# Kernel tuning notes

Hardware: AMD Instinct MI355X
Metric: run time of the kernel (lower is better)

The kernel has to match this reference:

```python
import jax, jax.numpy as jnp
import numpy as np

B, TAPE, N, F = 128, 100000, 50000, 32

def setup_inputs() -> dict:
    key = jax.random.key(0)
    k1, k2, k3, k4 = jax.random.split(key, 4)
    tape = jax.random.normal(k1, (B, TAPE), dtype=jnp.float32)
    input_indices = jax.random.randint(k2, (N, F), 0, TAPE)
    # He init scaled by fan-in, padding slots (index==0) zeroed as in __init__
    weights = jax.random.normal(k3, (N, F), dtype=jnp.float32) * jnp.sqrt(2.0 / F)
    weights = jnp.where(input_indices == 0, 0.0, weights)
    bias = jnp.zeros((N,), dtype=jnp.float32)
    output_indices = jnp.arange(N)
    act_type = jax.random.randint(k4, (N,), 0, 2)
    return {"tape": tape, "weights": weights, "bias": bias,
            "input_indices": input_indices, "output_indices": output_indices,
            "act_type": act_type}

def reference(tape, weights, bias, input_indices, output_indices, act_type):
    # gather padded fan-in inputs: [B, N, F]
    gathered = tape[:, input_indices]
    # weighted sum over fan-in + bias: [B, N]
    x = jnp.einsum('bnf,nf->bn', gathered, weights) + bias
    # per-activation-type apply (two activation groups: relu / tanh)
    x = jnp.where(act_type == 0, jax.nn.relu(x), jnp.tanh(x))
    # scatter results back into tape
    return tape.at[:, output_indices].set(x)
```

## Files before the change

kernel.cpp:

```cpp
#include <hip/hip_runtime.h>
#include <cmath>

#define TAPE_SZ 100000
#define N_SZ    50000
#define F_SZ    32
#define B_SZ    128
#define NGRP    8
#define GSUB    16
#define NBV     64
#define NCHUNK  ((N_SZ + NBV - 1) / NBV)
#define NGATHER (NCHUNK * NGRP)
#define NTAIL   512
#define TAIL_F4 1600000

static __device__ __forceinline__ unsigned short f32_to_bf16(float f) {
    unsigned int u = __float_as_uint(f);
    u = (u + 0x7fffu + ((u >> 16) & 1u)) >> 16;
    return (unsigned short)u;
}

__global__ __launch_bounds__(256) void transpose_tape(const float* __restrict__ in,
                                                      unsigned short* __restrict__ outT) {
    __shared__ float tile[32][129];
    const int x0 = blockIdx.x * 32;
    const int tx = threadIdx.x;
    const int ty = threadIdx.y;

    #pragma unroll
    for (int yy = ty; yy < B_SZ; yy += 8)
        tile[tx][yy] = in[(size_t)yy * TAPE_SZ + x0 + tx];
    __syncthreads();

    const int tid = ty * 32 + tx;
    const int g = tid >> 5;
    const int l = tid & 31;
    unsigned short* dst = outT + ((size_t)g * TAPE_SZ + x0 + l) * GSUB;
    union { unsigned short u[8]; uint4 q; } p0, p1;
    #pragma unroll
    for (int k = 0; k < 8; ++k) {
        p0.u[k] = f32_to_bf16(tile[l][g * GSUB + k]);
        p1.u[k] = f32_to_bf16(tile[l][g * GSUB + 8 + k]);
    }
    *(uint4*)dst       = p0.q;
    *(uint4*)(dst + 8) = p1.q;
}

__global__ __launch_bounds__(256, 8) void gather_mm(const unsigned short* __restrict__ tapeT,
                                                    const float* __restrict__ weights,
                                                    const float* __restrict__ bias,
                                                    const int*   __restrict__ in_idx,
                                                    const int*   __restrict__ out_idx,
                                                    const int*   __restrict__ act_type,
                                                    const float* __restrict__ tape,
                                                    float* __restrict__ out) {
    __shared__ int2  s_iw[NBV][33];
    __shared__ float s_bias[NBV];
    __shared__ int   s_act[NBV];
    __shared__ int   s_oidx[NBV];
    float (*s_x)[68] = (float (*)[68])&s_iw[0][0];

    const int tid = threadIdx.x;

    if (blockIdx.x >= NGATHER) {
        const float4* src = (const float4*)tape;
        float4*       dst = (float4*)out;
        const int stride = NTAIL * 256;
        for (int i = (blockIdx.x - NGATHER) * 256 + tid; i < TAIL_F4; i += stride) {
            const int b = i / 12500;
            const int j = i - b * 12500;
            const int off = b * (TAPE_SZ / 4) + (N_SZ / 4) + j;
            dst[off] = src[off];
        }
        return;
    }

    const int g     = blockIdx.x & (NGRP - 1);
    const int chunk = blockIdx.x >> 3;
    const int n0    = chunk * NBV;
    const int nend  = min(NBV, N_SZ - n0);

    for (int t = tid; t < nend * 32; t += 256) {
        const int n = t >> 5, f = t & 31;
        s_iw[n][f] = make_int2(in_idx[(size_t)n0 * 32 + t],
                               __float_as_int(weights[(size_t)n0 * 32 + t]));
    }
    if (tid < nend) {
        s_bias[tid] = bias[n0 + tid];
        s_act[tid]  = act_type[n0 + tid];
        s_oidx[tid] = out_idx[n0 + tid];
    }
    __syncthreads();

    const int nl = tid >> 2;
    const int q  = tid & 3;
    const unsigned short* tg = tapeT + (size_t)g * TAPE_SZ * GSUB + q * 4;

    float a0 = 0.f, a1 = 0.f, a2 = 0.f, a3 = 0.f;
    if (nl < nend) {
        #pragma unroll
        for (int fo = 0; fo < 32; fo += 8) {
            int2 iw8[8];
            #pragma unroll
            for (int j = 0; j < 8; ++j) iw8[j] = s_iw[nl][fo + j];
            uint2 q8[8];
            #pragma unroll
            for (int j = 0; j < 8; ++j)
                q8[j] = *(const uint2*)(tg + (size_t)iw8[j].x * GSUB);
            #pragma unroll
            for (int j = 0; j < 8; ++j) {
                const float w = __int_as_float(iw8[j].y);
                a0 = fmaf(__uint_as_float(q8[j].x << 16),         w, a0);
                a1 = fmaf(__uint_as_float(q8[j].x & 0xffff0000u), w, a1);
                a2 = fmaf(__uint_as_float(q8[j].y << 16),         w, a2);
                a3 = fmaf(__uint_as_float(q8[j].y & 0xffff0000u), w, a3);
            }
        }
        const float bz = s_bias[nl];
        a0 += bz; a1 += bz; a2 += bz; a3 += bz;
        if (s_act[nl] == 0) {
            a0 = fmaxf(a0, 0.f); a1 = fmaxf(a1, 0.f);
            a2 = fmaxf(a2, 0.f); a3 = fmaxf(a3, 0.f);
        } else {
            a0 = tanhf(a0); a1 = tanhf(a1); a2 = tanhf(a2); a3 = tanhf(a3);
        }
    }
    __syncthreads();

    if (nl < nend) {
        const int bs = q * 4;
        s_x[bs + 0][nl] = a0; s_x[bs + 1][nl] = a1;
        s_x[bs + 2][nl] = a2; s_x[bs + 3][nl] = a3;
    }
    __syncthreads();

    const int quads = (nend + 3) >> 2;
    for (int idx = tid; idx < GSUB * quads; idx += 256) {
        int bsub, j4;
        if (nend == NBV) { bsub = idx >> 4; j4 = idx & 15; }
        else             { bsub = idx / quads; j4 = idx - bsub * quads; }
        const int nq  = j4 * 4;
        const int oc0 = s_oidx[nq];
        float* orow = out + (size_t)(g * GSUB + bsub) * TAPE_SZ;
        const bool consec = (nq + 3 < nend) &&
                            (s_oidx[nq + 1] == oc0 + 1) &&
                            (s_oidx[nq + 2] == oc0 + 2) &&
                            (s_oidx[nq + 3] == oc0 + 3) && ((oc0 & 3) == 0);
        if (consec) {
            *(float4*)(orow + oc0) = make_float4(s_x[bsub][nq + 0], s_x[bsub][nq + 1],
                                                 s_x[bsub][nq + 2], s_x[bsub][nq + 3]);
        } else {
            #pragma unroll
            for (int c = 0; c < 4; ++c)
                if (nq + c < nend) orow[s_oidx[nq + c]] = s_x[bsub][nq + c];
        }
    }
}

__global__ __launch_bounds__(128) void gather_fallback(const float* __restrict__ tape,
                                                       const float* __restrict__ weights,
                                                       const float* __restrict__ bias,
                                                       const int*   __restrict__ in_idx,
                                                       const int*   __restrict__ out_idx,
                                                       const int*   __restrict__ act_type,
                                                       float* __restrict__ out) {
    const int n = blockIdx.x;
    const int b = threadIdx.x;
    float acc = 0.f;
    for (int f = 0; f < F_SZ; ++f) {
        acc += tape[(size_t)b * TAPE_SZ + in_idx[(size_t)n * F_SZ + f]] *
               weights[(size_t)n * F_SZ + f];
    }
    acc += bias[n];
    acc = (act_type[n] == 0) ? fmaxf(acc, 0.f) : tanhf(acc);
    out[(size_t)b * TAPE_SZ + out_idx[n]] = acc;
}

__global__ __launch_bounds__(256) void copy_tail_fb(const float* __restrict__ tape,
                                                    float* __restrict__ out) {
    const int n4 = (TAPE_SZ - N_SZ) / 4;
    int i = blockIdx.x * blockDim.x + threadIdx.x;
    int b = blockIdx.y;
    if (i < n4) {
        const float4* src = (const float4*)(tape + (size_t)b * TAPE_SZ + N_SZ);
        float4*       dst = (float4*)(out  + (size_t)b * TAPE_SZ + N_SZ);
        dst[i] = src[i];
    }
}

extern "C" void kernel_launch(void* const* d_in, const int* in_sizes, int n_in,
                              void* d_out, int out_size, void* d_ws, size_t ws_size,
                              hipStream_t stream) {
    const float* tape    = (const float*)d_in[0];
    const float* weights = (const float*)d_in[1];
    const float* bias    = (const float*)d_in[2];
    const int*   in_idx  = (const int*)d_in[3];
    const int*   out_idx = (const int*)d_in[4];
    const int*   act     = (const int*)d_in[5];
    float*       out     = (float*)d_out;

    const size_t need = (size_t)TAPE_SZ * B_SZ * sizeof(unsigned short);
    if (ws_size >= need) {
        unsigned short* tapeT = (unsigned short*)d_ws;
        transpose_tape<<<dim3(TAPE_SZ / 32), dim3(32, 8), 0, stream>>>(tape, tapeT);
        gather_mm<<<dim3(NGATHER + NTAIL), dim3(256), 0, stream>>>(
            tapeT, weights, bias, in_idx, out_idx, act, tape, out);
    } else {
        copy_tail_fb<<<dim3(((TAPE_SZ - N_SZ) / 4 + 255) / 256, B_SZ), 256, 0, stream>>>(tape, out);
        gather_fallback<<<dim3(N_SZ), 128, 0, stream>>>(
            tape, weights, bias, in_idx, out_idx, act, out);
    }
}
```

Baseline: 187.8 us.

## Add full-batch bf16 tape layout and split neurons between two gather schemes

The transpose now writes two bf16 copies of the tape: the existing batch-grouped layout and a neuron-major layout holding all 128 batch entries per tape slot. Neurons below a split point keep the grouped 64-neuron scheme. The rest use a new 16-neuron-per-block scheme that reads 16-byte full-batch rows with nontemporal loads and interleaves block types in the grid. The tail copy uses nontemporal loads and stores. The aim is to balance gather traffic and cut redundant index and weight loads, at the cost of a second transpose write, twice the workspace, and a hard-coded split ratio.

```diff
diff --git a/kernel.cpp b/kernel.cpp
--- a/kernel.cpp
+++ b/kernel.cpp
@@ -7,11 +7,19 @@
 #define B_SZ    128
 #define NGRP    8
 #define GSUB    16
+
 #define NBV     64
-#define NCHUNK  ((N_SZ + NBV - 1) / NBV)
-#define NGATHER (NCHUNK * NGRP)
+#define N_SPLIT 30016
+#define NCHA    (N_SPLIT / NBV)
+#define NB_B    16
+#define NBLK_B  ((N_SZ - N_SPLIT) / NB_B)
+#define NPER    157
+#define NMAIN   (NPER * 4 * 8)
 #define NTAIL   512
 #define TAIL_F4 1600000
+
+typedef float        f32x4 __attribute__((ext_vector_type(4)));
+typedef unsigned int u32x4 __attribute__((ext_vector_type(4)));
 
 static __device__ __forceinline__ unsigned short f32_to_bf16(float f) {
     unsigned int u = __float_as_uint(f);
@@ -19,8 +27,9 @@
     return (unsigned short)u;
 }
 
-__global__ __launch_bounds__(256) void transpose_tape(const float* __restrict__ in,
-                                                      unsigned short* __restrict__ outT) {
+__global__ __launch_bounds__(256) void transpose_both(const float* __restrict__ in,
+                                                      unsigned short* __restrict__ outP,
+                                                      unsigned short* __restrict__ outF) {
     __shared__ float tile[32][129];
     const int x0 = blockIdx.x * 32;
     const int tx = threadIdx.x;
@@ -32,76 +41,106 @@
     __syncthreads();
 
     const int tid = ty * 32 + tx;
-    const int g = tid >> 5;
-    const int l = tid & 31;
-    unsigned short* dst = outT + ((size_t)g * TAPE_SZ + x0 + l) * GSUB;
-    union { unsigned short u[8]; uint4 q; } p0, p1;
-    #pragma unroll
-    for (int k = 0; k < 8; ++k) {
-        p0.u[k] = f32_to_bf16(tile[l][g * GSUB + k]);
-        p1.u[k] = f32_to_bf16(tile[l][g * GSUB + 8 + k]);
-    }
-    *(uint4*)dst       = p0.q;
-    *(uint4*)(dst + 8) = p1.q;
-}
-
-__global__ __launch_bounds__(256, 8) void gather_mm(const unsigned short* __restrict__ tapeT,
-                                                    const float* __restrict__ weights,
-                                                    const float* __restrict__ bias,
-                                                    const int*   __restrict__ in_idx,
-                                                    const int*   __restrict__ out_idx,
-                                                    const int*   __restrict__ act_type,
-                                                    const float* __restrict__ tape,
-                                                    float* __restrict__ out) {
-    __shared__ int2  s_iw[NBV][33];
-    __shared__ float s_bias[NBV];
-    __shared__ int   s_act[NBV];
-    __shared__ int   s_oidx[NBV];
-    float (*s_x)[68] = (float (*)[68])&s_iw[0][0];
-
+    {
+        const int g = tid >> 5, l = tid & 31;
+        unsigned short* dst = outP + ((size_t)g * TAPE_SZ + x0 + l) * GSUB;
+        union { unsigned short u[8]; uint4 q; } p0, p1;
+        #pragma unroll
+        for (int k = 0; k < 8; ++k) {
+            p0.u[k] = f32_to_bf16(tile[l][g * GSUB + k]);
+            p1.u[k] = f32_to_bf16(tile[l][g * GSUB + 8 + k]);
+        }
+        *(uint4*)dst       = p0.q;
+        *(uint4*)(dst + 8) = p1.q;
+    }
+    {
+        const int l = tid >> 3, o = tid & 7;
+        unsigned short* dst = outF + (size_t)(x0 + l) * B_SZ + o * 8;
+        union { unsigned short u[8]; uint4 q; } p0, p1;
+        #pragma unroll
+        for (int k = 0; k < 8; ++k) {
+            p0.u[k] = f32_to_bf16(tile[l][o * 8 + k]);
+            p1.u[k] = f32_to_bf16(tile[l][64 + o * 8 + k]);
+        }
+        *(uint4*)dst        = p0.q;
+        *(uint4*)(dst + 64) = p1.q;
+    }
+}
+
+union SMem {
+    struct {
+        int2  iw[NBV][33];
+        float bias[NBV];
+        int   act[NBV];
+        int   oidx[NBV];
+    } a;
+    float ax[GSUB][68];
+    struct {
+        int   idx[NB_B][33];
+        float w[NB_B][33];
+        float x[NB_B][132];
+        float bias[NB_B];
+        int   act[NB_B];
+        int   oidx[NB_B];
+    } b;
+};
+
+__global__ __launch_bounds__(256) void gather_mm(const unsigned short* __restrict__ tapeP,
+                                                 const unsigned short* __restrict__ tapeF,
+                                                 const float* __restrict__ weights,
+                                                 const float* __restrict__ bias,
+                                                 const int*   __restrict__ in_idx,
+                                                 const int*   __restrict__ out_idx,
+                                                 const int*   __restrict__ act_type,
+                                                 const float* __restrict__ tape,
+                                                 float* __restrict__ out) {
+    __shared__ SMem sm;
     const int tid = threadIdx.x;
 
-    if (blockIdx.x >= NGATHER) {
-        const float4* src = (const float4*)tape;
-        float4*       dst = (float4*)out;
+    if (blockIdx.x >= NMAIN) {
         const int stride = NTAIL * 256;
-        for (int i = (blockIdx.x - NGATHER) * 256 + tid; i < TAIL_F4; i += stride) {
-            const int b = i / 12500;
-            const int j = i - b * 12500;
-            const int off = b * (TAPE_SZ / 4) + (N_SZ / 4) + j;
-            dst[off] = src[off];
+        for (int i = (blockIdx.x - NMAIN) * 256 + tid; i < TAIL_F4; i += stride) {
+            const int bb = i / 12500;
+            const int j = i - bb * 12500;
+            const size_t off = (size_t)bb * (TAPE_SZ / 4) + (N_SZ / 4) + j;
+            f32x4 v = __builtin_nontemporal_load((const f32x4*)tape + off);
+            __builtin_nontemporal_store(v, (f32x4*)out + off);
         }
         return;
     }
 
-    const int g     = blockIdx.x & (NGRP - 1);
-    const int chunk = blockIdx.x >> 3;
-    const int n0    = chunk * NBV;
-    const int nend  = min(NBV, N_SZ - n0);
-
-    for (int t = tid; t < nend * 32; t += 256) {
-        const int n = t >> 5, f = t & 31;
-        s_iw[n][f] = make_int2(in_idx[(size_t)n0 * 32 + t],
-                               __float_as_int(weights[(size_t)n0 * 32 + t]));
-    }
-    if (tid < nend) {
-        s_bias[tid] = bias[n0 + tid];
-        s_act[tid]  = act_type[n0 + tid];
-        s_oidx[tid] = out_idx[n0 + tid];
-    }
-    __syncthreads();
-
-    const int nl = tid >> 2;
-    const int q  = tid & 3;
-    const unsigned short* tg = tapeT + (size_t)g * TAPE_SZ * GSUB + q * 4;
-
-    float a0 = 0.f, a1 = 0.f, a2 = 0.f, a3 = 0.f;
-    if (nl < nend) {
+    const int oct = blockIdx.x >> 3;
+    const int g   = blockIdx.x & 7;
+    const int po  = oct & 3;
+    const int ro  = oct >> 2;
+
+    if (po < 3) {
+        const int chunk = ro * 3 + po;
+        if (chunk >= NCHA) return;
+        const int n0 = chunk * NBV;
+
+        for (int t = tid; t < NBV * 32; t += 256) {
+            const int n = t >> 5, f = t & 31;
+            sm.a.iw[n][f] = make_int2(in_idx[(size_t)n0 * 32 + t],
+                                      __float_as_int(weights[(size_t)n0 * 32 + t]));
+        }
+        if (tid < NBV) {
+            sm.a.bias[tid] = bias[n0 + tid];
+            sm.a.act[tid]  = act_type[n0 + tid];
+            sm.a.oidx[tid] = out_idx[n0 + tid];
+        }
+        __syncthreads();
+
+        const int nl = tid >> 2;
+        const int q  = tid & 3;
+        const unsigned short* tg = tapeP + (size_t)g * TAPE_SZ * GSUB + q * 4;
+
+        float a0 = 0.f, a1 = 0.f, a2 = 0.f, a3 = 0.f;
         #pragma unroll
         for (int fo = 0; fo < 32; fo += 8) {
             int2 iw8[8];
             #pragma unroll
-            for (int j = 0; j < 8; ++j) iw8[j] = s_iw[nl][fo + j];
+            for (int j = 0; j < 8; ++j) iw8[j] = sm.a.iw[nl][fo + j];
             uint2 q8[8];
             #pragma unroll
             for (int j = 0; j < 8; ++j)
@@ -115,6 +154,216 @@
                 a3 = fmaf(__uint_as_float(q8[j].y & 0xffff0000u), w, a3);
             }
         }
+        const float bz = sm.a.bias[nl];
+        a0 += bz; a1 += bz; a2 += bz; a3 += bz;
+        if (sm.a.act[nl] == 0) {
+            a0 = fmaxf(a0, 0.f); a1 = fmaxf(a1, 0.f);
+            a2 = fmaxf(a2, 0.f); a3 = fmaxf(a3, 0.f);
+        } else {
+            a0 = tanhf(a0); a1 = tanhf(a1); a2 = tanhf(a2); a3 = tanhf(a3);
+        }
+        __syncthreads();
+
+        {
+            const int bs = q * 4;
+            sm.ax[bs + 0][nl] = a0; sm.ax[bs + 1][nl] = a1;
+            sm.ax[bs + 2][nl] = a2; sm.ax[bs + 3][nl] = a3;
+        }
+        __syncthreads();
+
+        for (int idx = tid; idx < GSUB * 16; idx += 256) {
+            const int bsub = idx >> 4, j4 = idx & 15;
+            const int nq  = j4 * 4;
+            const int oc0 = sm.a.oidx[nq];
+            float* orow = out + (size_t)(g * GSUB + bsub) * TAPE_SZ;
+            const bool consec = (sm.a.oidx[nq + 1] == oc0 + 1) &&
+                                (sm.a.oidx[nq + 2] == oc0 + 2) &&
+                                (sm.a.oidx[nq + 3] == oc0 + 3) && ((oc0 & 3) == 0);
+            if (consec) {
+                *(float4*)(orow + oc0) = make_float4(sm.ax[bsub][nq + 0], sm.ax[bsub][nq + 1],
+                                                     sm.ax[bsub][nq + 2], sm.ax[bsub][nq + 3]);
+            } else {
+                #pragma unroll
+                for (int c = 0; c < 4; ++c)
+                    orow[sm.a.oidx[nq + c]] = sm.ax[bsub][nq + c];
+            }
+        }
+        return;
+    }
+
+    const int bidx = ro * 8 + g;
+    if (bidx >= NBLK_B) return;
+    const int n0 = N_SPLIT + bidx * NB_B;
+
+    for (int t = tid; t < NB_B * 32; t += 256) {
+        const int n = t >> 5, f = t & 31;
+        sm.b.idx[n][f] = in_idx[(size_t)n0 * 32 + t];
+        sm.b.w[n][f]   = weights[(size_t)n0 * 32 + t];
+    }
+    if (tid < NB_B) {
+        sm.b.bias[tid] = bias[n0 + tid];
+        sm.b.act[tid]  = act_type[n0 + tid];
+        sm.b.oidx[tid] = out_idx[n0 + tid];
+    }
+    __syncthreads();
+
+    const int nl = tid >> 4;
+    const int bx = tid & 15;
+    const unsigned short* tf = tapeF + bx * 8;
+    float a0 = 0.f, a1 = 0.f, a2 = 0.f, a3 = 0.f, a4 = 0.f, a5 = 0.f, a6 = 0.f, a7 = 0.f;
+
+    #pragma unroll
+    for (int fo = 0; fo < 32; fo += 8) {
+        int   i8[8]; float w8[8];
+        #pragma unroll
+        for (int j = 0; j < 8; ++j) { i8[j] = sm.b.idx[nl][fo + j]; w8[j] = sm.b.w[nl][fo + j]; }
+        u32x4 q8[8];
+        #pragma unroll
+        for (int j = 0; j < 8; ++j)
+            q8[j] = __builtin_nontemporal_load((const u32x4*)(tf + (size_t)i8[j] * B_SZ));
+        #pragma unroll
+        for (int j = 0; j < 8; ++j) {
+            const float w = w8[j];
+            a0 = fmaf(__uint_as_float(q8[j][0] << 16),         w, a0);
+            a1 = fmaf(__uint_as_float(q8[j][0] & 0xffff0000u), w, a1);
+            a2 = fmaf(__uint_as_float(q8[j][1] << 16),         w, a2);
+            a3 = fmaf(__uint_as_float(q8[j][1] & 0xffff0000u), w, a3);
+            a4 = fmaf(__uint_as_float(q8[j][2] << 16),         w, a4);
+            a5 = fmaf(__uint_as_float(q8[j][2] & 0xffff0000u), w, a5);
+            a6 = fmaf(__uint_as_float(q8[j][3] << 16),         w, a6);
+            a7 = fmaf(__uint_as_float(q8[j][3] & 0xffff0000u), w, a7);
+        }
+    }
+
+    const float bz = sm.b.bias[nl];
+    a0 += bz; a1 += bz; a2 += bz; a3 += bz; a4 += bz; a5 += bz; a6 += bz; a7 += bz;
+    if (sm.b.act[nl] == 0) {
+        a0 = fmaxf(a0, 0.f); a1 = fmaxf(a1, 0.f); a2 = fmaxf(a2, 0.f); a3 = fmaxf(a3, 0.f);
+        a4 = fmaxf(a4, 0.f); a5 = fmaxf(a5, 0.f); a6 = fmaxf(a6, 0.f); a7 = fmaxf(a7, 0.f);
+    } else {
+        a0 = tanhf(a0); a1 = tanhf(a1); a2 = tanhf(a2); a3 = tanhf(a3);
+        a4 = tanhf(a4); a5 = tanhf(a5); a6 = tanhf(a6); a7 = tanhf(a7);
+    }
+    {
+        const int b8 = bx * 8;
+        sm.b.x[nl][b8 + 0] = a0; sm.b.x[nl][b8 + 1] = a1; sm.b.x[nl][b8 + 2] = a2; sm.b.x[nl][b8 + 3] = a3;
+        sm.b.x[nl][b8 + 4] = a4; sm.b.x[nl][b8 + 5] = a5; sm.b.x[nl][b8 + 6] = a6; sm.b.x[nl][b8 + 7] = a7;
+    }
+    __syncthreads();
+
+    const int g4 = tid >> 6;
+    const int b0 = tid & 63;
+    const int oc0 = sm.b.oidx[g4 * 4];
+    const bool consec = (sm.b.oidx[g4 * 4 + 1] == oc0 + 1) &&
+                        (sm.b.oidx[g4 * 4 + 2] == oc0 + 2) &&
+                        (sm.b.oidx[g4 * 4 + 3] == oc0 + 3) && ((oc0 & 3) == 0);
+    #pragma unroll
+    for (int rep = 0; rep < 2; ++rep) {
+        const int b = b0 + rep * 64;
+        const float4 v = make_float4(sm.b.x[g4 * 4 + 0][b], sm.b.x[g4 * 4 + 1][b],
+                                     sm.b.x[g4 * 4 + 2][b], sm.b.x[g4 * 4 + 3][b]);
+        if (consec) {
+            *(float4*)(out + (size_t)b * TAPE_SZ + oc0) = v;
+        } else {
+            out[(size_t)b * TAPE_SZ + sm.b.oidx[g4 * 4 + 0]] = v.x;
+            out[(size_t)b * TAPE_SZ + sm.b.oidx[g4 * 4 + 1]] = v.y;
+            out[(size_t)b * TAPE_SZ + sm.b.oidx[g4 * 4 + 2]] = v.z;
+            out[(size_t)b * TAPE_SZ + sm.b.oidx[g4 * 4 + 3]] = v.w;
+        }
+    }
+}
+
+#define NBV2    64
+#define NCHUNK2 ((N_SZ + NBV2 - 1) / NBV2)
+#define NGATH2  (NCHUNK2 * NGRP)
+
+__global__ __launch_bounds__(256) void transpose_part(const float* __restrict__ in,
+                                                      unsigned short* __restrict__ outT) {
+    __shared__ float tile[32][129];
+    const int x0 = blockIdx.x * 32;
+    const int tx = threadIdx.x, ty = threadIdx.y;
+    #pragma unroll
+    for (int yy = ty; yy < B_SZ; yy += 8)
+        tile[tx][yy] = in[(size_t)yy * TAPE_SZ + x0 + tx];
+    __syncthreads();
+    const int tid = ty * 32 + tx;
+    const int g = tid >> 5, l = tid & 31;
+    unsigned short* dst = outT + ((size_t)g * TAPE_SZ + x0 + l) * GSUB;
+    union { unsigned short u[8]; uint4 q; } p0, p1;
+    #pragma unroll
+    for (int k = 0; k < 8; ++k) {
+        p0.u[k] = f32_to_bf16(tile[l][g * GSUB + k]);
+        p1.u[k] = f32_to_bf16(tile[l][g * GSUB + 8 + k]);
+    }
+    *(uint4*)dst = p0.q; *(uint4*)(dst + 8) = p1.q;
+}
+
+__global__ __launch_bounds__(256, 8) void gather_mm_part(const unsigned short* __restrict__ tapeT,
+                                                         const float* __restrict__ weights,
+                                                         const float* __restrict__ bias,
+                                                         const int*   __restrict__ in_idx,
+                                                         const int*   __restrict__ out_idx,
+                                                         const int*   __restrict__ act_type,
+                                                         const float* __restrict__ tape,
+                                                         float* __restrict__ out) {
+    __shared__ int2  s_iw[NBV2][33];
+    __shared__ float s_bias[NBV2];
+    __shared__ int   s_act[NBV2];
+    __shared__ int   s_oidx[NBV2];
+    float (*s_x)[68] = (float (*)[68])&s_iw[0][0];
+    const int tid = threadIdx.x;
+
+    if (blockIdx.x >= NGATH2) {
+        const float4* src = (const float4*)tape;
+        float4*       dst = (float4*)out;
+        const int stride = NTAIL * 256;
+        for (int i = (blockIdx.x - NGATH2) * 256 + tid; i < TAIL_F4; i += stride) {
+            const int b = i / 12500;
+            const int j = i - b * 12500;
+            const int off = b * (TAPE_SZ / 4) + (N_SZ / 4) + j;
+            dst[off] = src[off];
+        }
+        return;
+    }
+    const int g = blockIdx.x & (NGRP - 1);
+    const int chunk = blockIdx.x >> 3;
+    const int n0 = chunk * NBV2;
+    const int nend = min(NBV2, N_SZ - n0);
+
+    for (int t = tid; t < nend * 32; t += 256) {
+        const int n = t >> 5, f = t & 31;
+        s_iw[n][f] = make_int2(in_idx[(size_t)n0 * 32 + t],
+                               __float_as_int(weights[(size_t)n0 * 32 + t]));
+    }
+    if (tid < nend) {
+        s_bias[tid] = bias[n0 + tid];
+        s_act[tid]  = act_type[n0 + tid];
+        s_oidx[tid] = out_idx[n0 + tid];
+    }
+    __syncthreads();
+
+    const int nl = tid >> 2, q = tid & 3;
+    const unsigned short* tg = tapeT + (size_t)g * TAPE_SZ * GSUB + q * 4;
+    float a0 = 0.f, a1 = 0.f, a2 = 0.f, a3 = 0.f;
+    if (nl < nend) {
+        #pragma unroll
+        for (int fo = 0; fo < 32; fo += 8) {
+            int2 iw8[8];
+            #pragma unroll
+            for (int j = 0; j < 8; ++j) iw8[j] = s_iw[nl][fo + j];
+            uint2 q8[8];
+            #pragma unroll
+            for (int j = 0; j < 8; ++j)
+                q8[j] = *(const uint2*)(tg + (size_t)iw8[j].x * GSUB);
+            #pragma unroll
+            for (int j = 0; j < 8; ++j) {
+                const float w = __int_as_float(iw8[j].y);
+                a0 = fmaf(__uint_as_float(q8[j].x << 16),         w, a0);
+                a1 = fmaf(__uint_as_float(q8[j].x & 0xffff0000u), w, a1);
+                a2 = fmaf(__uint_as_float(q8[j].y << 16),         w, a2);
+                a3 = fmaf(__uint_as_float(q8[j].y & 0xffff0000u), w, a3);
+            }
+        }
         const float bz = s_bias[nl];
         a0 += bz; a1 += bz; a2 += bz; a3 += bz;
         if (s_act[nl] == 0) {
@@ -125,25 +374,22 @@
         }
     }
     __syncthreads();
-
     if (nl < nend) {
         const int bs = q * 4;
         s_x[bs + 0][nl] = a0; s_x[bs + 1][nl] = a1;
         s_x[bs + 2][nl] = a2; s_x[bs + 3][nl] = a3;
     }
     __syncthreads();
-
     const int quads = (nend + 3) >> 2;
     for (int idx = tid; idx < GSUB * quads; idx += 256) {
         int bsub, j4;
-        if (nend == NBV) { bsub = idx >> 4; j4 = idx & 15; }
-        else             { bsub = idx / quads; j4 = idx - bsub * quads; }
-        const int nq  = j4 * 4;
+        if (nend == NBV2) { bsub = idx >> 4; j4 = idx & 15; }
+        else              { bsub = idx / quads; j4 = idx - bsub * quads; }
+        const int nq = j4 * 4;
         const int oc0 = s_oidx[nq];
         float* orow = out + (size_t)(g * GSUB + bsub) * TAPE_SZ;
         const bool consec = (nq + 3 < nend) &&
-                            (s_oidx[nq + 1] == oc0 + 1) &&
-                            (s_oidx[nq + 2] == oc0 + 2) &&
+                            (s_oidx[nq + 1] == oc0 + 1) && (s_oidx[nq + 2] == oc0 + 2) &&
                             (s_oidx[nq + 3] == oc0 + 3) && ((oc0 & 3) == 0);
         if (consec) {
             *(float4*)(orow + oc0) = make_float4(s_x[bsub][nq + 0], s_x[bsub][nq + 1],
@@ -198,11 +444,17 @@
     const int*   act     = (const int*)d_in[5];
     float*       out     = (float*)d_out;
 
-    const size_t need = (size_t)TAPE_SZ * B_SZ * sizeof(unsigned short);
-    if (ws_size >= need) {
+    const size_t one = (size_t)TAPE_SZ * B_SZ * sizeof(unsigned short);
+    if (ws_size >= 2 * one) {
+        unsigned short* tapeP = (unsigned short*)d_ws;
+        unsigned short* tapeF = tapeP + (size_t)TAPE_SZ * B_SZ;
+        transpose_both<<<dim3(TAPE_SZ / 32), dim3(32, 8), 0, stream>>>(tape, tapeP, tapeF);
+        gather_mm<<<dim3(NMAIN + NTAIL), dim3(256), 0, stream>>>(
+            tapeP, tapeF, weights, bias, in_idx, out_idx, act, tape, out);
+    } else if (ws_size >= one) {
         unsigned short* tapeT = (unsigned short*)d_ws;
-        transpose_tape<<<dim3(TAPE_SZ / 32), dim3(32, 8), 0, stream>>>(tape, tapeT);
-        gather_mm<<<dim3(NGATHER + NTAIL), dim3(256), 0, stream>>>(
+        transpose_part<<<dim3(TAPE_SZ / 32), dim3(32, 8), 0, stream>>>(tape, tapeT);
+        gather_mm_part<<<dim3(NGATH2 + NTAIL), dim3(256), 0, stream>>>(
             tapeT, weights, bias, in_idx, out_idx, act, tape, out);
     } else {
         copy_tail_fb<<<dim3(((TAPE_SZ - N_SZ) / 4 + 255) / 256, B_SZ), 256, 0, stream>>>(tape, out);
```

Result: slower. 204.5 us (+8.9%).

## Add cooperative phased gather kernel with tape-range sorted indices and grid syncs

Applied to the files above, without the earlier changes.

Adds a new path that transposes the tape into a row-major bf16 layout (128 batch values per tape column), then launches a cooperative kernel. Each block sorts its neurons' fan-in indices into four tape-index ranges and processes one range at a time, with grid-wide syncs between ranges, so all blocks touch the same quarter of the table together and that quarter can stay in cache. Each thread now loads 64 contiguous bytes per index and accumulates 32 batch values, and the tail copy is folded into the same kernel. The cost is three grid barriers, heavy register use (32 accumulators, 4 blocks/CU) and a 782-block grid that must be fully co-resident; the kernel falls back to the old path if the cooperative launch fails.

```diff
diff --git a/kernel.cpp b/kernel.cpp
--- a/kernel.cpp
+++ b/kernel.cpp
@@ -1,15 +1,17 @@
 #include <hip/hip_runtime.h>
+#include <hip/hip_cooperative_groups.h>
 #include <cmath>
+
+namespace cg = cooperative_groups;
 
 #define TAPE_SZ 100000
 #define N_SZ    50000
 #define F_SZ    32
 #define B_SZ    128
-#define NGRP    8
-#define GSUB    16
-#define NBV     64
-#define NCHUNK  ((N_SZ + NBV - 1) / NBV)
-#define NGATHER (NCHUNK * NGRP)
+#define RANGE   25000
+#define NBV     128
+#define NCHUNK  391
+#define GRID_G  (NCHUNK*2)
 #define NTAIL   512
 #define TAIL_F4 1600000
 
@@ -19,8 +21,8 @@
     return (unsigned short)u;
 }
 
-__global__ __launch_bounds__(256) void transpose_tape(const float* __restrict__ in,
-                                                      unsigned short* __restrict__ outT) {
+__global__ __launch_bounds__(256) void transpose_full(const float* __restrict__ in,
+                                                      unsigned short* __restrict__ outF) {
     __shared__ float tile[32][129];
     const int x0 = blockIdx.x * 32;
     const int tx = threadIdx.x;
@@ -32,8 +34,184 @@
     __syncthreads();
 
     const int tid = ty * 32 + tx;
-    const int g = tid >> 5;
-    const int l = tid & 31;
+    const int l = tid >> 3, o = tid & 7;
+    unsigned short* dst = outF + (size_t)(x0 + l) * B_SZ + o * 8;
+    union { unsigned short u[8]; uint4 q; } p0, p1;
+    #pragma unroll
+    for (int k = 0; k < 8; ++k) {
+        p0.u[k] = f32_to_bf16(tile[l][o * 8 + k]);
+        p1.u[k] = f32_to_bf16(tile[l][64 + o * 8 + k]);
+    }
+    *(uint4*)dst        = p0.q;
+    *(uint4*)(dst + 64) = p1.q;
+}
+
+__global__ __launch_bounds__(256, 4) void gather_phased(
+    const unsigned short* __restrict__ tapeF,
+    const float* __restrict__ weights,
+    const float* __restrict__ bias,
+    const int*   __restrict__ in_idx,
+    const int*   __restrict__ out_idx,
+    const int*   __restrict__ act_type,
+    const float* __restrict__ tape,
+    float* __restrict__ out) {
+    __shared__ union {
+        struct {
+            uint2 ent[NBV][33];
+            int   start[NBV][5];
+        } s;
+        float x[64][132];
+    } u;
+    __shared__ int   s_oidx[NBV];
+    __shared__ float s_bias[NBV];
+    __shared__ int   s_act[NBV];
+
+    const int tid   = threadIdx.x;
+    const int h     = blockIdx.x & 1;
+    const int chunk = blockIdx.x >> 1;
+    const int n0    = chunk * NBV;
+    const int nend  = min(NBV, N_SZ - n0);
+
+    if (tid < NBV) {
+        if (tid < nend) {
+            const int*   ip = in_idx  + (size_t)(n0 + tid) * 32;
+            const float* wp = weights + (size_t)(n0 + tid) * 32;
+            int ix[32];
+            #pragma unroll
+            for (int f = 0; f < 32; ++f) ix[f] = ip[f];
+            int c0 = 0, c1 = 0, c2 = 0, c3 = 0;
+            #pragma unroll
+            for (int f = 0; f < 32; ++f) {
+                const int r = ix[f] / RANGE;
+                c0 += (r == 0); c1 += (r == 1); c2 += (r == 2); c3 += (r == 3);
+            }
+            int o0 = 0, o1 = c0, o2 = c0 + c1, o3 = c0 + c1 + c2;
+            u.s.start[tid][0] = 0;  u.s.start[tid][1] = o1;
+            u.s.start[tid][2] = o2; u.s.start[tid][3] = o3;
+            u.s.start[tid][4] = 32;
+            #pragma unroll
+            for (int f = 0; f < 32; ++f) {
+                const int r = ix[f] / RANGE;
+                int pos;
+                if      (r == 0) pos = o0++;
+                else if (r == 1) pos = o1++;
+                else if (r == 2) pos = o2++;
+                else             pos = o3++;
+                u.s.ent[tid][pos] = make_uint2((unsigned)ix[f], __float_as_uint(wp[f]));
+            }
+            s_oidx[tid] = out_idx[n0 + tid];
+            s_bias[tid] = bias[n0 + tid];
+            s_act[tid]  = act_type[n0 + tid];
+        } else {
+            #pragma unroll
+            for (int r = 0; r < 5; ++r) u.s.start[tid][r] = 0;
+        }
+    }
+    __syncthreads();
+
+    const int nl = tid >> 1;
+    const int bq = tid & 1;
+    const unsigned short* tg = tapeF + h * 64 + bq * 32;
+
+    float a[32];
+    #pragma unroll
+    for (int j = 0; j < 32; ++j) a[j] = 0.f;
+
+    cg::grid_group grid = cg::this_grid();
+
+    #pragma unroll 1
+    for (int r = 0; r < 4; ++r) {
+        const int e0 = u.s.start[nl][r];
+        const int e1 = u.s.start[nl][r + 1];
+        for (int e = e0; e < e1; ++e) {
+            const uint2 iw = u.s.ent[nl][e];
+            const unsigned short* p = tg + (size_t)iw.x * B_SZ;
+            const uint4 q0 = *(const uint4*)(p +  0);
+            const uint4 q1 = *(const uint4*)(p +  8);
+            const uint4 q2 = *(const uint4*)(p + 16);
+            const uint4 q3 = *(const uint4*)(p + 24);
+            const float wv = __uint_as_float(iw.y);
+#define ACC8(Q, B0) \
+            a[B0+0] = fmaf(__uint_as_float((Q).x << 16),          wv, a[B0+0]); \
+            a[B0+1] = fmaf(__uint_as_float((Q).x & 0xffff0000u),  wv, a[B0+1]); \
+            a[B0+2] = fmaf(__uint_as_float((Q).y << 16),          wv, a[B0+2]); \
+            a[B0+3] = fmaf(__uint_as_float((Q).y & 0xffff0000u),  wv, a[B0+3]); \
+            a[B0+4] = fmaf(__uint_as_float((Q).z << 16),          wv, a[B0+4]); \
+            a[B0+5] = fmaf(__uint_as_float((Q).z & 0xffff0000u),  wv, a[B0+5]); \
+            a[B0+6] = fmaf(__uint_as_float((Q).w << 16),          wv, a[B0+6]); \
+            a[B0+7] = fmaf(__uint_as_float((Q).w & 0xffff0000u),  wv, a[B0+7]);
+            ACC8(q0, 0) ACC8(q1, 8) ACC8(q2, 16) ACC8(q3, 24)
+#undef ACC8
+        }
+        if (r < 3) grid.sync();
+    }
+
+    {
+        const float bz = (nl < nend) ? s_bias[nl] : 0.f;
+        const int   at = (nl < nend) ? s_act[nl]  : 0;
+        #pragma unroll
+        for (int j = 0; j < 32; ++j) {
+            const float v = a[j] + bz;
+            a[j] = (at == 0) ? fmaxf(v, 0.f) : tanhf(v);
+        }
+    }
+    __syncthreads();
+    if (nl < nend) {
+        #pragma unroll
+        for (int j = 0; j < 32; ++j)
+            u.x[bq * 32 + j][nl] = a[j];
+    }
+    __syncthreads();
+
+    const int quads = (nend + 3) >> 2;
+    for (int it = tid; it < 64 * quads; it += 256) {
+        int bsub, j4;
+        if (nend == NBV) { bsub = it >> 5; j4 = it & 31; }
+        else             { bsub = it / quads; j4 = it - bsub * quads; }
+        const int nq  = j4 * 4;
+        const int oc0 = s_oidx[nq];
+        float* orow = out + (size_t)(h * 64 + bsub) * TAPE_SZ;
+        const bool consec = (nq + 3 < nend) &&
+                            (s_oidx[nq + 1] == oc0 + 1) &&
+                            (s_oidx[nq + 2] == oc0 + 2) &&
+                            (s_oidx[nq + 3] == oc0 + 3) && ((oc0 & 3) == 0);
+        if (consec) {
+            *(float4*)(orow + oc0) = *(const float4*)&u.x[bsub][nq];
+        } else {
+            #pragma unroll
+            for (int c = 0; c < 4; ++c)
+                if (nq + c < nend) orow[s_oidx[nq + c]] = u.x[bsub][nq + c];
+        }
+    }
+
+    {
+        const int stride = GRID_G * 256;
+        for (int i = blockIdx.x * 256 + tid; i < TAIL_F4; i += stride) {
+            const int bb = i / 12500;
+            const int j  = i - bb * 12500;
+            const size_t off = (size_t)bb * (TAPE_SZ / 4) + (N_SZ / 4) + j;
+            ((float4*)out)[off] = ((const float4*)tape)[off];
+        }
+    }
+}
+
+#define NGRP    8
+#define GSUB    16
+#define NBV2    64
+#define NCHUNK2 ((N_SZ + NBV2 - 1) / NBV2)
+#define NGATH2  (NCHUNK2 * NGRP)
+
+__global__ __launch_bounds__(256) void transpose_part(const float* __restrict__ in,
+                                                      unsigned short* __restrict__ outT) {
+    __shared__ float tile[32][129];
+    const int x0 = blockIdx.x * 32;
+    const int tx = threadIdx.x, ty = threadIdx.y;
+    #pragma unroll
+    for (int yy = ty; yy < B_SZ; yy += 8)
+        tile[tx][yy] = in[(size_t)yy * TAPE_SZ + x0 + tx];
+    __syncthreads();
+    const int tid = ty * 32 + tx;
+    const int g = tid >> 5, l = tid & 31;
     unsigned short* dst = outT + ((size_t)g * TAPE_SZ + x0 + l) * GSUB;
     union { unsigned short u[8]; uint4 q; } p0, p1;
     #pragma unroll
@@ -41,31 +219,29 @@
         p0.u[k] = f32_to_bf16(tile[l][g * GSUB + k]);
         p1.u[k] = f32_to_bf16(tile[l][g * GSUB + 8 + k]);
     }
-    *(uint4*)dst       = p0.q;
-    *(uint4*)(dst + 8) = p1.q;
-}
-
-__global__ __launch_bounds__(256, 8) void gather_mm(const unsigned short* __restrict__ tapeT,
-                                                    const float* __restrict__ weights,
-                                                    const float* __restrict__ bias,
-                                                    const int*   __restrict__ in_idx,
-                                                    const int*   __restrict__ out_idx,
-                                                    const int*   __restrict__ act_type,
-                                                    const float* __restrict__ tape,
-                                                    float* __restrict__ out) {
-    __shared__ int2  s_iw[NBV][33];
-    __shared__ float s_bias[NBV];
-    __shared__ int   s_act[NBV];
-    __shared__ int   s_oidx[NBV];
+    *(uint4*)dst = p0.q; *(uint4*)(dst + 8) = p1.q;
+}
+
+__global__ __launch_bounds__(256, 8) void gather_mm_part(const unsigned short* __restrict__ tapeT,
+                                                         const float* __restrict__ weights,
+                                                         const float* __restrict__ bias,
+                                                         const int*   __restrict__ in_idx,
+                                                         const int*   __restrict__ out_idx,
+                                                         const int*   __restrict__ act_type,
+                                                         const float* __restrict__ tape,
+                                                         float* __restrict__ out) {
+    __shared__ int2  s_iw[NBV2][33];
+    __shared__ float s_bias[NBV2];
+    __shared__ int   s_act[NBV2];
+    __shared__ int   s_oidx[NBV2];
     float (*s_x)[68] = (float (*)[68])&s_iw[0][0];
-
     const int tid = threadIdx.x;
 
-    if (blockIdx.x >= NGATHER) {
+    if (blockIdx.x >= NGATH2) {
         const float4* src = (const float4*)tape;
         float4*       dst = (float4*)out;
         const int stride = NTAIL * 256;
-        for (int i = (blockIdx.x - NGATHER) * 256 + tid; i < TAIL_F4; i += stride) {
+        for (int i = (blockIdx.x - NGATH2) * 256 + tid; i < TAIL_F4; i += stride) {
             const int b = i / 12500;
             const int j = i - b * 12500;
             const int off = b * (TAPE_SZ / 4) + (N_SZ / 4) + j;
@@ -73,11 +249,10 @@
         }
         return;
     }
-
-    const int g     = blockIdx.x & (NGRP - 1);
+    const int g = blockIdx.x & (NGRP - 1);
     const int chunk = blockIdx.x >> 3;
-    const int n0    = chunk * NBV;
-    const int nend  = min(NBV, N_SZ - n0);
+    const int n0 = chunk * NBV2;
+    const int nend = min(NBV2, N_SZ - n0);
 
     for (int t = tid; t < nend * 32; t += 256) {
         const int n = t >> 5, f = t & 31;
@@ -91,10 +266,8 @@
     }
     __syncthreads();
 
-    const int nl = tid >> 2;
-    const int q  = tid & 3;
+    const int nl = tid >> 2, q = tid & 3;
     const unsigned short* tg = tapeT + (size_t)g * TAPE_SZ * GSUB + q * 4;
-
     float a0 = 0.f, a1 = 0.f, a2 = 0.f, a3 = 0.f;
     if (nl < nend) {
         #pragma unroll
@@ -125,25 +298,22 @@
         }
     }
     __syncthreads();
-
     if (nl < nend) {
         const int bs = q * 4;
         s_x[bs + 0][nl] = a0; s_x[bs + 1][nl] = a1;
         s_x[bs + 2][nl] = a2; s_x[bs + 3][nl] = a3;
     }
     __syncthreads();
-
     const int quads = (nend + 3) >> 2;
     for (int idx = tid; idx < GSUB * quads; idx += 256) {
         int bsub, j4;
-        if (nend == NBV) { bsub = idx >> 4; j4 = idx & 15; }
-        else             { bsub = idx / quads; j4 = idx - bsub * quads; }
-        const int nq  = j4 * 4;
+        if (nend == NBV2) { bsub = idx >> 4; j4 = idx & 15; }
+        else              { bsub = idx / quads; j4 = idx - bsub * quads; }
+        const int nq = j4 * 4;
         const int oc0 = s_oidx[nq];
         float* orow = out + (size_t)(g * GSUB + bsub) * TAPE_SZ;
         const bool consec = (nq + 3 < nend) &&
-                            (s_oidx[nq + 1] == oc0 + 1) &&
-                            (s_oidx[nq + 2] == oc0 + 2) &&
+                            (s_oidx[nq + 1] == oc0 + 1) && (s_oidx[nq + 2] == oc0 + 2) &&
                             (s_oidx[nq + 3] == oc0 + 3) && ((oc0 & 3) == 0);
         if (consec) {
             *(float4*)(orow + oc0) = make_float4(s_x[bsub][nq + 0], s_x[bsub][nq + 1],
@@ -198,11 +368,25 @@
     const int*   act     = (const int*)d_in[5];
     float*       out     = (float*)d_out;
 
-    const size_t need = (size_t)TAPE_SZ * B_SZ * sizeof(unsigned short);
-    if (ws_size >= need) {
+    const size_t one = (size_t)TAPE_SZ * B_SZ * sizeof(unsigned short);
+    if (ws_size >= 2 * one) {
+        unsigned short* tapeF = (unsigned short*)d_ws;
+        transpose_full<<<dim3(TAPE_SZ / 32), dim3(32, 8), 0, stream>>>(tape, tapeF);
+        void* args[] = {(void*)&tapeF, (void*)&weights, (void*)&bias, (void*)&in_idx,
+                        (void*)&out_idx, (void*)&act, (void*)&tape, (void*)&out};
+        hipError_t e = hipLaunchCooperativeKernel((const void*)gather_phased,
+                                                  dim3(GRID_G), dim3(256),
+                                                  args, 0, stream);
+        if (e != hipSuccess) {
+            unsigned short* tapeP = tapeF + (size_t)TAPE_SZ * B_SZ;
+            transpose_part<<<dim3(TAPE_SZ / 32), dim3(32, 8), 0, stream>>>(tape, tapeP);
+            gather_mm_part<<<dim3(NGATH2 + NTAIL), dim3(256), 0, stream>>>(
+                tapeP, weights, bias, in_idx, out_idx, act, tape, out);
+        }
+    } else if (ws_size >= one) {
         unsigned short* tapeT = (unsigned short*)d_ws;
-        transpose_tape<<<dim3(TAPE_SZ / 32), dim3(32, 8), 0, stream>>>(tape, tapeT);
-        gather_mm<<<dim3(NGATHER + NTAIL), dim3(256), 0, stream>>>(
+        transpose_part<<<dim3(TAPE_SZ / 32), dim3(32, 8), 0, stream>>>(tape, tapeT);
+        gather_mm_part<<<dim3(NGATH2 + NTAIL), dim3(256), 0, stream>>>(
             tapeT, weights, bias, in_idx, out_idx, act, tape, out);
     } else {
         copy_tail_fb<<<dim3(((TAPE_SZ - N_SZ) / 4 + 255) / 256, B_SZ), 256, 0, stream>>>(tape, out);
```

After: 479.8 us. 156% more time.

## Widen batch groups to 64, bucket gather indices by tape range, fuse tail copy

Applied to the files above, without the earlier changes.

The bf16 transposed tape now groups 64 batch rows per tape column instead of 16, so each gathered index fetches 128 contiguous bytes and each thread accumulates 16 batch values. The gather kernel uses 512 threads and 128 nodes per block, and sorts each node's 32 fan-in entries into four tape-range buckets. All threads sweep the buckets in step with a barrier between them, which aims to improve L2 locality. The untouched tail columns are now copied from the transpose kernel's shared tile, so the separate tail-copy blocks are gone. In exchange the gather kernel needs more registers and extra barriers, and the fan-in is split across 4 rounds of scattered loads.

```diff
diff --git a/kernel.cpp b/kernel.cpp
--- a/kernel.cpp
+++ b/kernel.cpp
@@ -5,13 +5,11 @@
 #define N_SZ    50000
 #define F_SZ    32
 #define B_SZ    128
-#define NGRP    8
-#define GSUB    16
-#define NBV     64
-#define NCHUNK  ((N_SZ + NBV - 1) / NBV)
-#define NGATHER (NCHUNK * NGRP)
-#define NTAIL   512
-#define TAIL_F4 1600000
+#define GSUB    64
+#define RANGE   25000
+#define NBV     128
+#define NCHUNK  391
+#define GRID_G  (NCHUNK*2)
 
 static __device__ __forceinline__ unsigned short f32_to_bf16(float f) {
     unsigned int u = __float_as_uint(f);
@@ -19,8 +17,9 @@
     return (unsigned short)u;
 }
 
-__global__ __launch_bounds__(256) void transpose_tape(const float* __restrict__ in,
-                                                      unsigned short* __restrict__ outT) {
+__global__ __launch_bounds__(256) void transpose_g64(const float* __restrict__ in,
+                                                     unsigned short* __restrict__ outG,
+                                                     float* __restrict__ out) {
     __shared__ float tile[32][129];
     const int x0 = blockIdx.x * 32;
     const int tx = threadIdx.x;
@@ -32,112 +31,143 @@
     __syncthreads();
 
     const int tid = ty * 32 + tx;
-    const int g = tid >> 5;
-    const int l = tid & 31;
-    unsigned short* dst = outT + ((size_t)g * TAPE_SZ + x0 + l) * GSUB;
+    const int l = tid >> 3;
+    const int o = tid & 7;
+    const int g = o >> 2;
+    const int j = o & 3;
+    unsigned short* dst = outG + ((size_t)g * TAPE_SZ + x0 + l) * GSUB + j * 16;
     union { unsigned short u[8]; uint4 q; } p0, p1;
     #pragma unroll
     for (int k = 0; k < 8; ++k) {
-        p0.u[k] = f32_to_bf16(tile[l][g * GSUB + k]);
-        p1.u[k] = f32_to_bf16(tile[l][g * GSUB + 8 + k]);
+        p0.u[k] = f32_to_bf16(tile[l][g * GSUB + j * 16 + k]);
+        p1.u[k] = f32_to_bf16(tile[l][g * GSUB + j * 16 + 8 + k]);
     }
     *(uint4*)dst       = p0.q;
     *(uint4*)(dst + 8) = p1.q;
-}
-
-__global__ __launch_bounds__(256, 8) void gather_mm(const unsigned short* __restrict__ tapeT,
-                                                    const float* __restrict__ weights,
-                                                    const float* __restrict__ bias,
-                                                    const int*   __restrict__ in_idx,
-                                                    const int*   __restrict__ out_idx,
-                                                    const int*   __restrict__ act_type,
-                                                    const float* __restrict__ tape,
-                                                    float* __restrict__ out) {
-    __shared__ int2  s_iw[NBV][33];
+
+    if (x0 + tx >= N_SZ) {
+        #pragma unroll
+        for (int yy = ty; yy < B_SZ; yy += 8)
+            out[(size_t)yy * TAPE_SZ + x0 + tx] = tile[tx][yy];
+    }
+}
+
+__global__ __launch_bounds__(512, 4) void gather_g64(
+    const unsigned short* __restrict__ tapeG,
+    const float* __restrict__ weights,
+    const float* __restrict__ bias,
+    const int*   __restrict__ in_idx,
+    const int*   __restrict__ out_idx,
+    const int*   __restrict__ act_type,
+    float* __restrict__ out) {
+    __shared__ union {
+        struct {
+            uint2 ent[NBV][33];
+            int   start[NBV][5];
+        } s;
+        float x[GSUB][132];
+    } u;
+    __shared__ int   s_oidx[NBV];
     __shared__ float s_bias[NBV];
     __shared__ int   s_act[NBV];
-    __shared__ int   s_oidx[NBV];
-    float (*s_x)[68] = (float (*)[68])&s_iw[0][0];
-
-    const int tid = threadIdx.x;
-
-    if (blockIdx.x >= NGATHER) {
-        const float4* src = (const float4*)tape;
-        float4*       dst = (float4*)out;
-        const int stride = NTAIL * 256;
-        for (int i = (blockIdx.x - NGATHER) * 256 + tid; i < TAIL_F4; i += stride) {
-            const int b = i / 12500;
-            const int j = i - b * 12500;
-            const int off = b * (TAPE_SZ / 4) + (N_SZ / 4) + j;
-            dst[off] = src[off];
-        }
-        return;
-    }
-
-    const int g     = blockIdx.x & (NGRP - 1);
-    const int chunk = blockIdx.x >> 3;
+
+    const int tid   = threadIdx.x;
+    const int g     = blockIdx.x & 1;
+    const int chunk = blockIdx.x >> 1;
     const int n0    = chunk * NBV;
     const int nend  = min(NBV, N_SZ - n0);
 
-    for (int t = tid; t < nend * 32; t += 256) {
-        const int n = t >> 5, f = t & 31;
-        s_iw[n][f] = make_int2(in_idx[(size_t)n0 * 32 + t],
-                               __float_as_int(weights[(size_t)n0 * 32 + t]));
-    }
-    if (tid < nend) {
-        s_bias[tid] = bias[n0 + tid];
-        s_act[tid]  = act_type[n0 + tid];
-        s_oidx[tid] = out_idx[n0 + tid];
+    if (tid < NBV) {
+        if (tid < nend) {
+            const int*   ip = in_idx  + (size_t)(n0 + tid) * 32;
+            const float* wp = weights + (size_t)(n0 + tid) * 32;
+            int ix[32];
+            #pragma unroll
+            for (int f = 0; f < 32; ++f) ix[f] = ip[f];
+            int c0 = 0, c1 = 0, c2 = 0, c3 = 0;
+            #pragma unroll
+            for (int f = 0; f < 32; ++f) {
+                const int r = ix[f] / RANGE;
+                c0 += (r == 0); c1 += (r == 1); c2 += (r == 2); c3 += (r == 3);
+            }
+            int o0 = 0, o1 = c0, o2 = c0 + c1, o3 = c0 + c1 + c2;
+            u.s.start[tid][0] = 0;  u.s.start[tid][1] = o1;
+            u.s.start[tid][2] = o2; u.s.start[tid][3] = o3;
+            u.s.start[tid][4] = 32;
+            #pragma unroll
+            for (int f = 0; f < 32; ++f) {
+                const int r = ix[f] / RANGE;
+                int pos;
+                if      (r == 0) pos = o0++;
+                else if (r == 1) pos = o1++;
+                else if (r == 2) pos = o2++;
+                else             pos = o3++;
+                u.s.ent[tid][pos] = make_uint2((unsigned)ix[f], __float_as_uint(wp[f]));
+            }
+            s_oidx[tid] = out_idx[n0 + tid];
+            s_bias[tid] = bias[n0 + tid];
+            s_act[tid]  = act_type[n0 + tid];
+        } else {
+            #pragma unroll
+            for (int r = 0; r < 5; ++r) u.s.start[tid][r] = 0;
+        }
     }
     __syncthreads();
 
     const int nl = tid >> 2;
     const int q  = tid & 3;
-    const unsigned short* tg = tapeT + (size_t)g * TAPE_SZ * GSUB + q * 4;
-
-    float a0 = 0.f, a1 = 0.f, a2 = 0.f, a3 = 0.f;
+    const unsigned short* tg = tapeG + (size_t)g * TAPE_SZ * GSUB + q * 16;
+
+    float a[16];
+    #pragma unroll
+    for (int k = 0; k < 16; ++k) a[k] = 0.f;
+
+    #pragma unroll 1
+    for (int r = 0; r < 4; ++r) {
+        const int e1 = u.s.start[nl][r + 1];
+        for (int e = u.s.start[nl][r]; e < e1; ++e) {
+            const uint2 iw = u.s.ent[nl][e];
+            const unsigned short* p = tg + (size_t)iw.x * GSUB;
+            const uint4 q0 = *(const uint4*)(p);
+            const uint4 q1 = *(const uint4*)(p + 8);
+            const float wv = __uint_as_float(iw.y);
+#define ACC8(Q, B0) \
+            a[B0+0] = fmaf(__uint_as_float((Q).x << 16),          wv, a[B0+0]); \
+            a[B0+1] = fmaf(__uint_as_float((Q).x & 0xffff0000u),  wv, a[B0+1]); \
+            a[B0+2] = fmaf(__uint_as_float((Q).y << 16),          wv, a[B0+2]); \
+            a[B0+3] = fmaf(__uint_as_float((Q).y & 0xffff0000u),  wv, a[B0+3]); \
+            a[B0+4] = fmaf(__uint_as_float((Q).z << 16),          wv, a[B0+4]); \
+            a[B0+5] = fmaf(__uint_as_float((Q).z & 0xffff0000u),  wv, a[B0+5]); \
+            a[B0+6] = fmaf(__uint_as_float((Q).w << 16),          wv, a[B0+6]); \
+            a[B0+7] = fmaf(__uint_as_float((Q).w & 0xffff0000u),  wv, a[B0+7]);
+            ACC8(q0, 0) ACC8(q1, 8)
+#undef ACC8
+        }
+        __syncthreads();
+    }
+
+    {
+        const float bz = (nl < nend) ? s_bias[nl] : 0.f;
+        const int   at = (nl < nend) ? s_act[nl]  : 0;
+        #pragma unroll
+        for (int k = 0; k < 16; ++k) {
+            const float v = a[k] + bz;
+            a[k] = (at == 0) ? fmaxf(v, 0.f) : tanhf(v);
+        }
+    }
+    __syncthreads();
     if (nl < nend) {
         #pragma unroll
-        for (int fo = 0; fo < 32; fo += 8) {
-            int2 iw8[8];
-            #pragma unroll
-            for (int j = 0; j < 8; ++j) iw8[j] = s_iw[nl][fo + j];
-            uint2 q8[8];
-            #pragma unroll
-            for (int j = 0; j < 8; ++j)
-                q8[j] = *(const uint2*)(tg + (size_t)iw8[j].x * GSUB);
-            #pragma unroll
-            for (int j = 0; j < 8; ++j) {
-                const float w = __int_as_float(iw8[j].y);
-                a0 = fmaf(__uint_as_float(q8[j].x << 16),         w, a0);
-                a1 = fmaf(__uint_as_float(q8[j].x & 0xffff0000u), w, a1);
-                a2 = fmaf(__uint_as_float(q8[j].y << 16),         w, a2);
-                a3 = fmaf(__uint_as_float(q8[j].y & 0xffff0000u), w, a3);
-            }
-        }
-        const float bz = s_bias[nl];
-        a0 += bz; a1 += bz; a2 += bz; a3 += bz;
-        if (s_act[nl] == 0) {
-            a0 = fmaxf(a0, 0.f); a1 = fmaxf(a1, 0.f);
-            a2 = fmaxf(a2, 0.f); a3 = fmaxf(a3, 0.f);
-        } else {
-            a0 = tanhf(a0); a1 = tanhf(a1); a2 = tanhf(a2); a3 = tanhf(a3);
-        }
-    }
-    __syncthreads();
-
-    if (nl < nend) {
-        const int bs = q * 4;
-        s_x[bs + 0][nl] = a0; s_x[bs + 1][nl] = a1;
-        s_x[bs + 2][nl] = a2; s_x[bs + 3][nl] = a3;
+        for (int k = 0; k < 16; ++k)
+            u.x[q * 16 + k][nl] = a[k];
     }
     __syncthreads();
 
     const int quads = (nend + 3) >> 2;
-    for (int idx = tid; idx < GSUB * quads; idx += 256) {
+    for (int it = tid; it < GSUB * quads; it += 512) {
         int bsub, j4;
-        if (nend == NBV) { bsub = idx >> 4; j4 = idx & 15; }
-        else             { bsub = idx / quads; j4 = idx - bsub * quads; }
+        if (nend == NBV) { bsub = it >> 5; j4 = it & 31; }
+        else             { bsub = it / quads; j4 = it - bsub * quads; }
         const int nq  = j4 * 4;
         const int oc0 = s_oidx[nq];
         float* orow = out + (size_t)(g * GSUB + bsub) * TAPE_SZ;
@@ -146,12 +176,11 @@
                             (s_oidx[nq + 2] == oc0 + 2) &&
                             (s_oidx[nq + 3] == oc0 + 3) && ((oc0 & 3) == 0);
         if (consec) {
-            *(float4*)(orow + oc0) = make_float4(s_x[bsub][nq + 0], s_x[bsub][nq + 1],
-                                                 s_x[bsub][nq + 2], s_x[bsub][nq + 3]);
+            *(float4*)(orow + oc0) = *(const float4*)&u.x[bsub][nq];
         } else {
             #pragma unroll
             for (int c = 0; c < 4; ++c)
-                if (nq + c < nend) orow[s_oidx[nq + c]] = s_x[bsub][nq + c];
+                if (nq + c < nend) orow[s_oidx[nq + c]] = u.x[bsub][nq + c];
         }
     }
 }
@@ -200,10 +229,10 @@
 
     const size_t need = (size_t)TAPE_SZ * B_SZ * sizeof(unsigned short);
     if (ws_size >= need) {
-        unsigned short* tapeT = (unsigned short*)d_ws;
-        transpose_tape<<<dim3(TAPE_SZ / 32), dim3(32, 8), 0, stream>>>(tape, tapeT);
-        gather_mm<<<dim3(NGATHER + NTAIL), dim3(256), 0, stream>>>(
-            tapeT, weights, bias, in_idx, out_idx, act, tape, out);
+        unsigned short* tapeG = (unsigned short*)d_ws;
+        transpose_g64<<<dim3(TAPE_SZ / 32), dim3(32, 8), 0, stream>>>(tape, tapeG, out);
+        gather_g64<<<dim3(GRID_G), dim3(512), 0, stream>>>(
+            tapeG, weights, bias, in_idx, out_idx, act, out);
     } else {
         copy_tail_fb<<<dim3(((TAPE_SZ - N_SZ) / 4 + 255) / 256, B_SZ), 256, 0, stream>>>(tape, out);
         gather_fallback<<<dim3(N_SZ), 128, 0, stream>>>(
```

After: 197.3 us. 1.05x slower.
